# Kernel tuning notes

Measured on AMD Instinct MI355X. Metric: run time of the kernel, lower is better.

Reference implementation:

```python
import jax, jax.numpy as jnp
from jax import lax
import numpy as np

B, T, N, HORIZON = 64, 12, 512, 12
IN_DIM = 1; OUT_DIM = 1; YCOV = 1
RNN = 64; MEM_NUM = 20; MEM_DIM = 64; EMB = 10; CHEB_K = 3
DEC_DIM = RNN + MEM_DIM  # 128


def _xavier(key, shape):
    fan_in, fan_out = shape[0], shape[-1]
    std = float(np.sqrt(2.0 / (fan_in + fan_out)))
    return jax.random.normal(key, shape, dtype=jnp.float32) * std


def _cheb_feats(A, x, batched):
    mm = (lambda a, v: jnp.einsum('bnm,bmc->bnc', a, v)) if batched else (lambda a, v: jnp.einsum('nm,bmc->bnc', a, v))
    gs = [x, mm(A, x)]
    for _ in range(CHEB_K - 2):
        gs.append(2.0 * mm(A, gs[-1]) - gs[-2])
    return jnp.concatenate(gs, axis=-1)


def _agcn(x, A, W, b, batched):
    return _cheb_feats(A, x, batched) @ W + b


def _cell(x, state, A, Wg, bg, Wu, bu, batched):
    # AGCRN GRU cell
    hid = state.shape[-1]
    inp = jnp.concatenate([x, state], axis=-1)
    z_r = jax.nn.sigmoid(_agcn(inp, A, Wg, bg, batched))
    z, r = z_r[..., :hid], z_r[..., hid:]
    cand = jnp.concatenate([x, z * state], axis=-1)
    hc = jnp.tanh(_agcn(cand, A, Wu, bu, batched))
    return r * state + (1.0 - r) * hc


def _encode(x, A, Wg, bg, Wu, bu):
    # x: [B,T,N,C] -> last hidden state [B,N,RNN]
    xt = jnp.swapaxes(x, 0, 1)  # [T,B,N,C]
    init = jnp.zeros((x.shape[0], x.shape[2], RNN), x.dtype)
    def step(state, xt_):
        h = _cell(xt_, state, A, Wg, bg, Wu, bu, batched=False)
        return h, None
    h_t, _ = lax.scan(step, init, xt)
    return h_t


def _query_memory(h_t, Memory, Wq):
    q = h_t @ Wq                                   # [B,N,mem_dim]
    att = jax.nn.softmax(q @ Memory.T, axis=-1)    # [B,N,mem_num]
    value = att @ Memory                           # [B,N,mem_dim]
    _, ind = lax.top_k(att, 2)
    pos = Memory[ind[..., 0]]                      # [B,N,mem_dim]
    return value, pos


def setup_inputs() -> dict:
    key = jax.random.key(0)
    ks = jax.random.split(key, 20)
    x = jax.random.normal(ks[0], (B, T, N, IN_DIM), dtype=jnp.float32)
    x_cov = jax.random.normal(ks[1], (B, T, N, 1), dtype=jnp.float32)
    x_his = jax.random.normal(ks[2], (B, T, N, IN_DIM), dtype=jnp.float32)
    y_cov = jax.random.normal(ks[3], (B, HORIZON, N, YCOV), dtype=jnp.float32)
    a = jax.random.uniform(ks[4], (N, N), dtype=jnp.float32)
    adj = a / jnp.sum(a, axis=-1, keepdims=True)
    enc_in = IN_DIM + RNN
    dec_in = OUT_DIM + YCOV + DEC_DIM
    return {
        'x': x, 'x_cov': x_cov, 'x_his': x_his, 'y_cov': y_cov, 'adj': adj,
        'enc_gate_W': _xavier(ks[5], (CHEB_K * enc_in, 2 * RNN)),
        'enc_gate_b': jnp.zeros((2 * RNN,), jnp.float32),
        'enc_upd_W': _xavier(ks[6], (CHEB_K * enc_in, RNN)),
        'enc_upd_b': jnp.zeros((RNN,), jnp.float32),
        'dec_gate_W': _xavier(ks[7], (CHEB_K * dec_in, 2 * DEC_DIM)),
        'dec_gate_b': jnp.zeros((2 * DEC_DIM,), jnp.float32),
        'dec_upd_W': _xavier(ks[8], (CHEB_K * dec_in, DEC_DIM)),
        'dec_upd_b': jnp.zeros((DEC_DIM,), jnp.float32),
        'Memory': _xavier(ks[9], (MEM_NUM, MEM_DIM)),
        'Wq': _xavier(ks[10], (RNN, MEM_DIM)),
        'hyper_W': _xavier(ks[11], (DEC_DIM, EMB)),
        'hyper_b': jnp.zeros((EMB,), jnp.float32),
        'lat_W': _xavier(ks[12], (MEM_DIM, 1)),
        'lat_b': jnp.zeros((1,), jnp.float32),
        'proj_W': _xavier(ks[13], (DEC_DIM, OUT_DIM)),
        'proj_b': jnp.zeros((OUT_DIM,), jnp.float32),
    }


def reference(x, x_cov, x_his, y_cov, adj,
              enc_gate_W, enc_gate_b, enc_upd_W, enc_upd_b,
              dec_gate_W, dec_gate_b, dec_upd_W, dec_upd_b,
              Memory, Wq, hyper_W, hyper_b, lat_W, lat_b, proj_W, proj_b):
    # --- encoder on x and x_his (shared weights, single static support) ---
    h_t = _encode(x, adj, enc_gate_W, enc_gate_b, enc_upd_W, enc_upd_b)
    h_att, pos = _query_memory(h_t, Memory, Wq)
    h_his_t = _encode(x_his, adj, enc_gate_W, enc_gate_b, enc_upd_W, enc_upd_b)
    _, pos_his = _query_memory(h_his_t, Memory, Wq)
    # schema==1 latent distance head (sigmoid activation)
    latent_dis = jax.nn.sigmoid(((pos - pos_his) @ lat_W + lat_b)[..., 0])  # [B,N]
    # --- adaptive decoder support from hypernetwork ---
    h_aug = jnp.concatenate([h_t, h_att], axis=-1)          # [B,N,DEC_DIM]
    node_emb = h_aug @ hyper_W + hyper_b                    # [B,N,EMB]
    support = jax.nn.softmax(jax.nn.relu(jnp.einsum('bnc,bmc->bnm', node_emb, node_emb)), axis=-1)  # [B,N,N]
    # --- decoder rollout (inference path, no teacher forcing) ---
    go0 = jnp.zeros((x.shape[0], N, OUT_DIM), x.dtype)
    ycov_t = jnp.swapaxes(y_cov, 0, 1)  # [HORIZON,B,N,YCOV]
    def dec_step(carry, yc):
        go, h = carry
        xt = jnp.concatenate([go, yc], axis=-1)
        h = _cell(xt, h, support, dec_gate_W, dec_gate_b, dec_upd_W, dec_upd_b, batched=True)
        go = h @ proj_W + proj_b
        return (go, h), go
    _, outs = lax.scan(dec_step, (go0, h_aug), ycov_t)
    output = jnp.swapaxes(outs, 0, 1)  # [B,HORIZON,N,OUT_DIM]
    return output, latent_dis
```

## Files before the change

### kernel.cpp

```cpp
#include <hip/hip_runtime.h>
#include <hip/hip_bf16.h>


typedef __attribute__((ext_vector_type(8))) short s8v;
typedef __attribute__((ext_vector_type(4))) float f4v;
typedef __attribute__((ext_vector_type(4))) unsigned short u4v;

__device__ __forceinline__ float b2f(unsigned short u){
  union{unsigned int i; float f;} v; v.i = ((unsigned int)u)<<16; return v.f;
}
__device__ __forceinline__ unsigned short f2b(float f){
  union{float f; unsigned int i;} v; v.f = f;
  unsigned int r = v.i + 0x7fff + ((v.i >> 16) & 1);
  return (unsigned short)(r >> 16);
}

__global__ void k_zero16(uint4* p, int n){
  int i = blockIdx.x*256 + threadIdx.x;
  if (i < n) p[i] = make_uint4(0,0,0,0);
}


__global__ void k_reorderF(const float* __restrict__ W, float* __restrict__ Wr,
                           int HC, int NEX, int SEGW, int J){
  int idx = blockIdx.x*256 + threadIdx.x;
  int K = 3*SEGW;
  if (idx >= K*J) return;
  int k = idx / J, j = idx - k*J;
  int seg = k / SEGW, c = k - seg*SEGW;
  int CIN = HC + NEX;
  float v = 0.f;
  if (c < HC)       v = W[(size_t)(seg*CIN + NEX + c)*J + j];
  else if (c < CIN) v = W[(size_t)(seg*CIN + (c-HC))*J + j];
  Wr[(size_t)k*J + j] = v;
}

__global__ __launch_bounds__(256) void k_a2e(const float* __restrict__ A,
                                             float* __restrict__ A2e){
  __shared__ __align__(16) float As[32][132];
  __shared__ __align__(16) float Bs[32][132];
  int t = threadIdx.x;
  int r0 = (blockIdx.x & 3) * 128;
  int c0 = (blockIdx.x >> 2) * 128;
  int tr = t & 15, tc = t >> 4;
  float acc[8][8];
  #pragma unroll
  for (int i=0;i<8;i++)
    #pragma unroll
    for (int j=0;j<8;j++) acc[i][j]=0.f;
  for (int k0=0;k0<512;k0+=32){
    #pragma unroll
    for (int i=0;i<4;i++){
      int s = t + i*256;
      int k = s & 31, rq = s >> 5;
      const float* ap = A + (size_t)(r0 + rq*4)*512 + k0 + k;
      float4 v;
      v.x = ap[0]; v.y = ap[512]; v.z = ap[1024]; v.w = ap[1536];
      *(float4*)&As[k][rq*4] = v;
    }
    #pragma unroll
    for (int i=0;i<4;i++){
      int s = t + i*256;
      int k = s >> 5, cq = s & 31;
      float4 v = *(const float4*)(A + (size_t)(k0+k)*512 + c0 + cq*4);
      *(float4*)&Bs[k][cq*4] = v;
    }
    __syncthreads();
    #pragma unroll 8
    for (int k=0;k<32;k++){
      float a[8], b[8];
      *(float4*)&a[0] = *(const float4*)&As[k][tr*4];
      *(float4*)&a[4] = *(const float4*)&As[k][64+tr*4];
      *(float4*)&b[0] = *(const float4*)&Bs[k][tc*4];
      *(float4*)&b[4] = *(const float4*)&Bs[k][64+tc*4];
      #pragma unroll
      for (int i=0;i<8;i++)
        #pragma unroll
        for (int j=0;j<8;j++) acc[i][j] += a[i]*b[j];
    }
    __syncthreads();
  }
  #pragma unroll
  for (int i=0;i<8;i++){
    int r = r0 + (i<4 ? tr*4+i : 64+tr*4+i-4);
    #pragma unroll
    for (int j=0;j<8;j++){
      int c = c0 + (j<4 ? tc*4+j : 64+tc*4+j-4);
      A2e[(size_t)r*512 + c] = 2.f*acc[i][j] - (r==c ? 1.f : 0.f);
    }
  }
}

template<int MODE>
__global__ __launch_bounds__(256) void k_enc(
    const float* __restrict__ A, const float* __restrict__ A2e,
    const float* __restrict__ hsrc,
    const float* __restrict__ xa, const float* __restrict__ xb,
    int tstep, const float* __restrict__ Wr, const float* __restrict__ bias,
    float* __restrict__ zh, float* __restrict__ rbuf, float* __restrict__ henc)
{
  constexpr int J  = (MODE==0) ? 128 : 64;
  constexpr int TN = (MODE==0) ? 8 : 4;
  __shared__ __align__(16) float R1[4352];
  __shared__ __align__(16) float F0t[2][65][66];
  float (*sA)[68]   = (float(*)[68])(R1);
  float (*sA2)[68]  = (float(*)[68])(R1 + 1088);
  float (*sB0)[68]  = (float(*)[68])(R1 + 2176);
  float (*sB1)[68]  = (float(*)[68])(R1 + 3264);
  float (*G12h)[66] = (float(*)[66])(R1);
  const int t = threadIdx.x;
  const int z = blockIdx.x;
  const int rowblk = blockIdx.z;
  const int n0 = rowblk * 64;
  const int tr = t & 15, tc = t >> 4;
  const int xrow = t & 63, xmat = (t >> 6) & 1, xbb = t >> 7;
  const float* xp0 = xa + ((size_t)z*12 + tstep)*512;
  const float* xp1 = xb + ((size_t)z*12 + tstep)*512;

  float acc[2][2][4][4];
  #pragma unroll
  for (int m=0;m<2;m++)
    #pragma unroll
    for (int b=0;b<2;b++)
      #pragma unroll
      for (int i=0;i<4;i++)
        #pragma unroll
        for (int j=0;j<4;j++) acc[m][b][i][j]=0.f;
  float xacc = 0.f;

  for (int k0=0;k0<512;k0+=16){
    {
      int k = t & 15, rq = t >> 4;
      const float* ap  = A   + (size_t)(n0 + rq*4)*512 + k0 + k;
      const float* a2p = A2e + (size_t)(n0 + rq*4)*512 + k0 + k;
      float4 v, w;
      v.x = ap[0];  v.y = ap[512];  v.z = ap[1024];  v.w = ap[1536];
      w.x = a2p[0]; w.y = a2p[512]; w.z = a2p[1024]; w.w = a2p[1536];
      *(float4*)&sA[k][rq*4]  = v;
      *(float4*)&sA2[k][rq*4] = w;
    }
    {
      int k = t >> 4, cq = t & 15;
      *(float4*)&sB0[k][cq*4] = *(const float4*)(hsrc + (size_t)(z*512 + k0 + k)*64 + cq*4);
      *(float4*)&sB1[k][cq*4] = *(const float4*)(hsrc + (size_t)((z+64)*512 + k0 + k)*64 + cq*4);
    }
    if (t < 16)      sB0[t][64]    = xp0[k0 + t];
    else if (t < 32) sB1[t-16][64] = xp1[k0 + t - 16];
    __syncthreads();
    #pragma unroll 4
    for (int k=0;k<16;k++){
      float a1[4], a2[4], b0[4], b1[4];
      *(float4*)&a1[0] = *(const float4*)&sA[k][tr*4];
      *(float4*)&a2[0] = *(const float4*)&sA2[k][tr*4];
      *(float4*)&b0[0] = *(const float4*)&sB0[k][tc*4];
      *(float4*)&b1[0] = *(const float4*)&sB1[k][tc*4];
      #pragma unroll
      for (int i=0;i<4;i++)
        #pragma unroll
        for (int j=0;j<4;j++){
          acc[0][0][i][j] += a1[i]*b0[j];
          acc[0][1][i][j] += a1[i]*b1[j];
          acc[1][0][i][j] += a2[i]*b0[j];
          acc[1][1][i][j] += a2[i]*b1[j];
        }
      float am = xmat ? sA2[k][xrow] : sA[k][xrow];
      xacc += am * (xbb ? sB1[k][64] : sB0[k][64]);
    }
    if ((k0 >> 6) == rowblk){
      const int off = k0 & 63;
      for (int s=t; s<2080; s+=256){
        int sb = (s >= 1040) ? 1 : 0;
        int ss = s - sb*1040;
        int c = ss >> 4, kk = ss & 15;
        F0t[sb][c][off + kk] = sb ? sB1[kk][c] : sB0[kk][c];
      }
    }
    __syncthreads();
  }

  for (int bbi=0; bbi<2; bbi++){
    #pragma unroll
    for (int j=0;j<4;j++){
      float4 v;
      v.x = acc[0][bbi][0][j]; v.y = acc[0][bbi][1][j];
      v.z = acc[0][bbi][2][j]; v.w = acc[0][bbi][3][j];
      *(float4*)&G12h[tc*4 + j][tr*4] = v;
    }
    if (xbb == bbi && xmat == 0) G12h[64][xrow] = xacc;
    __syncthreads();

    float acc2[4][TN];
    #pragma unroll
    for (int i=0;i<4;i++)
      #pragma unroll
      for (int jj=0;jj<TN;jj++) acc2[i][jj]=0.f;
    const int j0 = tc*TN;

    #pragma unroll 4
    for (int c=0;c<65;c++){
      float a[4], w[TN];
      *(float4*)&a[0] = *(const float4*)&F0t[bbi][c][tr*4];
      #pragma unroll
      for (int q=0;q<TN;q+=4) *(float4*)&w[q] = *(const float4*)(Wr + (size_t)c*J + j0 + q);
      #pragma unroll
      for (int i=0;i<4;i++)
        #pragma unroll
        for (int jj=0;jj<TN;jj++) acc2[i][jj] += a[i]*w[jj];
    }
    #pragma unroll 4
    for (int c=0;c<65;c++){
      float a[4], w[TN];
      *(float4*)&a[0] = *(const float4*)&G12h[c][tr*4];
      #pragma unroll
      for (int q=0;q<TN;q+=4) *(float4*)&w[q] = *(const float4*)(Wr + (size_t)(68+c)*J + j0 + q);
      #pragma unroll
      for (int i=0;i<4;i++)
        #pragma unroll
        for (int jj=0;jj<TN;jj++) acc2[i][jj] += a[i]*w[jj];
    }
    __syncthreads();
    #pragma unroll
    for (int j=0;j<4;j++){
      float4 v;
      v.x = acc[1][bbi][0][j]; v.y = acc[1][bbi][1][j];
      v.z = acc[1][bbi][2][j]; v.w = acc[1][bbi][3][j];
      *(float4*)&G12h[tc*4 + j][tr*4] = v;
    }
    if (xbb == bbi && xmat == 1) G12h[64][xrow] = xacc;
    __syncthreads();
    #pragma unroll 4
    for (int c=0;c<65;c++){
      float a[4], w[TN];
      *(float4*)&a[0] = *(const float4*)&G12h[c][tr*4];
      #pragma unroll
      for (int q=0;q<TN;q+=4) *(float4*)&w[q] = *(const float4*)(Wr + (size_t)(136+c)*J + j0 + q);
      #pragma unroll
      for (int i=0;i<4;i++)
        #pragma unroll
        for (int jj=0;jj<TN;jj++) acc2[i][jj] += a[i]*w[jj];
    }

    float bj[TN];
    #pragma unroll
    for (int jj=0;jj<TN;jj++) bj[jj] = bias[j0+jj];
    const int gbase = (z + bbi*64)*512 + n0;
    #pragma unroll
    for (int i=0;i<4;i++){
      const int lr = tr*4 + i;
      const int row = gbase + lr;
      if (MODE == 0){
        float s[8];
        #pragma unroll
        for (int jj=0;jj<TN;jj++) s[jj] = 1.f/(1.f + __expf(-(acc2[i][jj] + bj[jj])));
        if (j0 < 64){
          float4 o0, o1;
          o0.x = s[0]*F0t[bbi][j0+0][lr]; o0.y = s[1]*F0t[bbi][j0+1][lr];
          o0.z = s[2]*F0t[bbi][j0+2][lr]; o0.w = s[3]*F0t[bbi][j0+3][lr];
          o1.x = s[4]*F0t[bbi][j0+4][lr]; o1.y = s[5]*F0t[bbi][j0+5][lr];
          o1.z = s[6]*F0t[bbi][j0+6][lr]; o1.w = s[7]*F0t[bbi][j0+7][lr];
          *(float4*)(zh + (size_t)row*64 + j0)     = o0;
          *(float4*)(zh + (size_t)row*64 + j0 + 4) = o1;
        } else {
          float4 o0, o1;
          o0.x=s[0]; o0.y=s[1]; o0.z=s[2]; o0.w=s[3];
          o1.x=s[4]; o1.y=s[5]; o1.z=s[6]; o1.w=s[7];
          *(float4*)(rbuf + (size_t)row*64 + j0 - 64) = o0;
          *(float4*)(rbuf + (size_t)row*64 + j0 - 60) = o1;
        }
      } else {
        float4 h4 = *(const float4*)(henc + (size_t)row*64 + j0);
        float4 r4 = *(const float4*)(rbuf + (size_t)row*64 + j0);
        float hv[4] = {h4.x,h4.y,h4.z,h4.w};
        float rv[4] = {r4.x,r4.y,r4.z,r4.w};
        float ov[4];
        #pragma unroll
        for (int jj=0;jj<4;jj++){
          float hc = 1.f - 2.f/(__expf(2.f*(acc2[i][jj] + bj[jj])) + 1.f);
          ov[jj] = rv[jj]*hv[jj] + (1.f - rv[jj])*hc;
        }
        float4 o; o.x=ov[0]; o.y=ov[1]; o.z=ov[2]; o.w=ov[3];
        *(float4*)(henc + (size_t)row*64 + j0) = o;
      }
    }
    __syncthreads();
  }
}


__global__ void k_reorderB(const float* __restrict__ W, unsigned short* __restrict__ Wr,
                           int HC, int NEX, int C, int KP, int J){
  int idx = blockIdx.x*256 + threadIdx.x;
  if (idx >= J*KP) return;
  int j = idx / KP, kp = idx - j*KP;
  float v = 0.f;
  if (kp < 3*C){
    int seg = kp / C, c = kp - seg*C;
    int CIN = HC + NEX;
    if (c < HC)       v = W[(size_t)(seg*CIN + NEX + c)*J + j];
    else if (c < CIN) v = W[(size_t)(seg*CIN + (c-HC))*J + j];
  }
  Wr[(size_t)j*KP + kp] = f2b(v);
}

__global__ __launch_bounds__(256) void k_sup2(const unsigned short* __restrict__ S,
                                              unsigned short* __restrict__ S2){
  __shared__ unsigned short Bs[128*40];
  const int t = threadIdx.x;
  const int w = t >> 6, L = t & 63, lm = L & 15, q = L >> 4;
  const int bb = blockIdx.z;
  const int n0 = blockIdx.x * 128;
  const int m0 = blockIdx.y * 128;
  const unsigned short* Sb = S + (size_t)bb * 262144;
  unsigned short* S2b = S2 + (size_t)bb * 262144;
  f4v acc[2][8];
  #pragma unroll
  for (int i=0;i<2;i++)
    #pragma unroll
    for (int j=0;j<8;j++)
      #pragma unroll
      for (int r=0;r<4;r++) acc[i][j][r] = 0.f;
  for (int k0=0;k0<512;k0+=32){
    #pragma unroll
    for (int i=0;i<2;i++){
      int s = t + i*256;
      int kk = s >> 4, mg = s & 15;
      s8v v = *(const s8v*)(Sb + (size_t)(k0+kk)*512 + m0 + mg*8);
      #pragma unroll
      for (int e=0;e<8;e++) Bs[(mg*8+e)*40 + kk] = ((unsigned short*)&v)[e];
    }
    __syncthreads();
    s8v a0 = *(const s8v*)(Sb + (size_t)(n0 + w*32 + lm)*512 + k0 + q*8);
    s8v a1 = *(const s8v*)(Sb + (size_t)(n0 + w*32 + 16 + lm)*512 + k0 + q*8);
    #pragma unroll
    for (int ct=0;ct<8;ct++){
      s8v b = *(const s8v*)&Bs[(ct*16+lm)*40 + q*8];
      acc[0][ct] = __builtin_amdgcn_mfma_f32_16x16x32_bf16(a0, b, acc[0][ct], 0,0,0);
      acc[1][ct] = __builtin_amdgcn_mfma_f32_16x16x32_bf16(a1, b, acc[1][ct], 0,0,0);
    }
    __syncthreads();
  }
  #pragma unroll
  for (int rt=0;rt<2;rt++){
    const int row = n0 + w*32 + rt*16 + q*4;
    #pragma unroll
    for (int ct=0;ct<8;ct++){
      const int col = m0 + ct*16 + lm;
      #pragma unroll
      for (int r=0;r<4;r++){
        float v = 2.f*acc[rt][ct][r] - ((row+r)==col ? 1.f : 0.f);
        S2b[(size_t)(row+r)*512 + col] = f2b(v);
      }
    }
  }
}

__global__ __launch_bounds__(256) void k_mmB2(
    const unsigned short* __restrict__ M1, const unsigned short* __restrict__ M2,
    unsigned short* fC, unsigned short* fR)
{
  constexpr int C = 144;
  __shared__ unsigned short Bs[C*40];
  const int t = threadIdx.x;
  const int w = t >> 6, L = t & 63, lm = L & 15, q = L >> 4;
  const int bb = blockIdx.z;
  const int n0 = blockIdx.x * 64;
  const unsigned short* M1b = M1 + (size_t)bb * 262144;
  const unsigned short* M2b = M2 + (size_t)bb * 262144;
  unsigned short* fCb = fC + (size_t)bb * 432 * 512;
  const unsigned short* Xb = fCb;
  unsigned short* O1 = fCb + (size_t)C * 512;
  unsigned short* O2 = fCb + (size_t)2 * C * 512;
  const int rw = n0 + w*16;

  f4v acc[2][9];
  #pragma unroll
  for (int i=0;i<2;i++)
    #pragma unroll
    for (int j=0;j<9;j++)
      #pragma unroll
      for (int r=0;r<4;r++) acc[i][j][r] = 0.f;

  s8v breg[3];
  const size_t ar = (size_t)(rw + lm)*512 + q*8;
  #pragma unroll
  for (int i=0;i<3;i++){
    int s = t + i*256;
    if (s < C*4) breg[i] = *(const s8v*)(Xb + (size_t)(s>>2)*512 + (s&3)*8);
  }
  s8v a1 = *(const s8v*)(M1b + ar);
  s8v a2 = *(const s8v*)(M2b + ar);

  for (int ks=0; ks<16; ks++){
    #pragma unroll
    for (int i=0;i<3;i++){
      int s = t + i*256;
      if (s < C*4) *(s8v*)&Bs[(s>>2)*40 + (s&3)*8] = breg[i];
    }
    __syncthreads();
    const int kn = (ks < 15) ? (ks+1)*32 : 0;
    #pragma unroll
    for (int i=0;i<3;i++){
      int s = t + i*256;
      if (s < C*4) breg[i] = *(const s8v*)(Xb + (size_t)(s>>2)*512 + kn + (s&3)*8);
    }
    s8v a1n = *(const s8v*)(M1b + ar + kn);
    s8v a2n = *(const s8v*)(M2b + ar + kn);
    #pragma unroll
    for (int ct=0; ct<9; ct++){
      s8v b = *(const s8v*)&Bs[(ct*16+lm)*40 + q*8];
      acc[0][ct] = __builtin_amdgcn_mfma_f32_16x16x32_bf16(a1, b, acc[0][ct], 0,0,0);
      acc[1][ct] = __builtin_amdgcn_mfma_f32_16x16x32_bf16(a2, b, acc[1][ct], 0,0,0);
    }
    __syncthreads();
    a1 = a1n; a2 = a2n;
  }
  const int m0 = rw + q*4;
  #pragma unroll
  for (int ct=0; ct<9; ct++){
    const int c = ct*16 + lm;
    u4v o1, o2;
    #pragma unroll
    for (int r=0;r<4;r++){ o1[r] = f2b(acc[0][ct][r]); o2[r] = f2b(acc[1][ct][r]); }
    *(u4v*)(O1 + (size_t)c*512 + m0) = o1;
    *(u4v*)(O2 + (size_t)c*512 + m0) = o2;
    const size_t rb = (size_t)(bb*512 + m0)*448;
    #pragma unroll
    for (int r=0;r<4;r++){
      fR[rb + (size_t)r*448 + 144 + c] = o1[r];
      fR[rb + (size_t)r*448 + 288 + c] = o2[r];
    }
  }
}

template<int KSTEPS, int JT16, int MODE, int HC>
__global__ __launch_bounds__(256) void k_gwB(
    unsigned short* fR, int KP,
    const unsigned short* __restrict__ Wr, const float* __restrict__ bias,
    unsigned short* fC, int C3,
    float* hC, float* rbuf)
{
  constexpr int JT = JT16*16;
  constexpr int BIT = JT*4/256;
  __shared__ unsigned short Bs[JT*40];
  const int t = threadIdx.x;
  const int w = t >> 6, L = t & 63, lm = L & 15, q = L >> 4;
  const int row0 = blockIdx.x * 128;
  const int j0 = blockIdx.y * JT;
  const int rw = row0 + w*32;

  f4v acc[2][JT16];
  #pragma unroll
  for (int i=0;i<2;i++)
    #pragma unroll
    for (int j=0;j<JT16;j++)
      #pragma unroll
      for (int r=0;r<4;r++) acc[i][j][r] = 0.f;

  s8v breg[BIT];
  const unsigned short* Wb = Wr + (size_t)j0*KP;
  const size_t ar0 = (size_t)(rw + lm)*KP + q*8;
  const size_t ar1 = (size_t)(rw + 16 + lm)*KP + q*8;

  #pragma unroll
  for (int i=0;i<BIT;i++){
    int s = t + i*256;
    breg[i] = *(const s8v*)(Wb + (size_t)(s>>2)*KP + (s&3)*8);
  }
  s8v a0 = *(const s8v*)(fR + ar0);
  s8v a1 = *(const s8v*)(fR + ar1);

  for (int ks=0; ks<KSTEPS; ks++){
    #pragma unroll
    for (int i=0;i<BIT;i++){
      int s = t + i*256;
      *(s8v*)&Bs[(s>>2)*40 + (s&3)*8] = breg[i];
    }
    __syncthreads();
    const int kn = (ks < KSTEPS-1) ? (ks+1)*32 : 0;
    #pragma unroll
    for (int i=0;i<BIT;i++){
      int s = t + i*256;
      breg[i] = *(const s8v*)(Wb + (size_t)(s>>2)*KP + kn + (s&3)*8);
    }
    s8v a0n = *(const s8v*)(fR + ar0 + kn);
    s8v a1n = *(const s8v*)(fR + ar1 + kn);
    #pragma unroll
    for (int ct=0; ct<JT16; ct++){
      s8v b = *(const s8v*)&Bs[(ct*16+lm)*40 + q*8];
      acc[0][ct] = __builtin_amdgcn_mfma_f32_16x16x32_bf16(a0, b, acc[0][ct], 0,0,0);
      acc[1][ct] = __builtin_amdgcn_mfma_f32_16x16x32_bf16(a1, b, acc[1][ct], 0,0,0);
    }
    __syncthreads();
    a0 = a0n; a1 = a1n;
  }
  #pragma unroll
  for (int rt=0; rt<2; rt++){
    const int m0 = rw + rt*16 + q*4;
    const int bb = m0 >> 9, n = m0 & 511;
    #pragma unroll
    for (int ct=0; ct<JT16; ct++){
      const int j = j0 + ct*16 + lm;
      const float bj = bias[j];
      if (MODE == 0){
        if (j < HC){
          f4v h4 = *(const f4v*)(hC + ((size_t)bb*HC + j)*512 + n);
          u4v o;
          #pragma unroll
          for (int r=0;r<4;r++){
            float s = 1.f/(1.f + __expf(-(acc[rt][ct][r] + bj)));
            float zh = s * h4[r];
            o[r] = f2b(zh);
            fR[(size_t)(m0+r)*KP + j] = o[r];
          }
          *(u4v*)(fC + ((size_t)bb*C3 + j)*512 + n) = o;
        } else {
          f4v rv;
          #pragma unroll
          for (int r=0;r<4;r++) rv[r] = 1.f/(1.f + __expf(-(acc[rt][ct][r] + bj)));
          *(f4v*)(rbuf + ((size_t)bb*HC + (j-HC))*512 + n) = rv;
        }
      } else {
        f4v h4 = *(const f4v*)(hC + ((size_t)bb*HC + j)*512 + n);
        f4v r4 = *(const f4v*)(rbuf + ((size_t)bb*HC + j)*512 + n);
        u4v o; f4v hn;
        #pragma unroll
        for (int r=0;r<4;r++){
          float e = __expf(2.f*(acc[rt][ct][r] + bj));
          float hc_ = 1.f - 2.f/(e + 1.f);
          hn[r] = r4[r]*h4[r] + (1.f - r4[r])*hc_;
          o[r] = f2b(hn[r]);
          fR[(size_t)(m0+r)*KP + j] = o[r];
        }
        *(f4v*)(hC + ((size_t)bb*HC + j)*512 + n) = hn;
        *(u4v*)(fC + ((size_t)bb*C3 + j)*512 + n) = o;
      }
    }
  }
}


__global__ void k_extras_dec(const float* __restrict__ yc,
    unsigned short* fR, unsigned short* fC, int tstep){
  int rr = blockIdx.x*256 + threadIdx.x;
  int bb = rr >> 9, n = rr & 511;
  unsigned short u = f2b(yc[((size_t)bb*12 + tstep)*512 + n]);
  fR[(size_t)rr*448 + 129] = u;
  fC[((size_t)bb*432 + 129)*512 + n] = u;
}
__global__ void k_fix_go(unsigned short* fR, unsigned short* fC){
  int rr = blockIdx.x*256 + threadIdx.x;
  int bb = rr >> 9, n = rr & 511;
  fR[(size_t)rr*448 + 128] = 0;
  fC[((size_t)bb*432 + 128)*512 + n] = 0;
}

__global__ __launch_bounds__(256) void k_query(const float* __restrict__ hR,
      const float* __restrict__ Wq, const float* __restrict__ Mem,
      float* __restrict__ hCd, unsigned short* fR, unsigned short* fC,
      int* __restrict__ it, int* __restrict__ ih){
  int sub = threadIdx.x >> 6, lane = threadIdx.x & 63;
  int row = blockIdx.x*4 + sub;
  __shared__ float sh[4][64], sq[4][64], ss[4][20];
  float hv = hR[(size_t)row*64 + lane];
  sh[sub][lane] = hv;
  __syncthreads();
  float qv = 0.f;
  for (int c=0;c<64;c++) qv += sh[sub][c]*Wq[c*64 + lane];
  sq[sub][lane] = qv;
  __syncthreads();
  if (lane < 20){
    float s = 0.f;
    for (int j=0;j<64;j++) s += sq[sub][j]*Mem[lane*64 + j];
    ss[sub][lane] = s;
  }
  __syncthreads();
  float mx = -1e30f; int am = 0;
  for (int m=0;m<20;m++){ float s = ss[sub][m]; if (s > mx){ mx = s; am = m; } }
  float sum = 0.f;
  for (int m=0;m<20;m++) sum += __expf(ss[sub][m]-mx);
  float inv = 1.f/sum;
  float v = 0.f;
  for (int m=0;m<20;m++) v += __expf(ss[sub][m]-mx)*inv*Mem[m*64 + lane];
  int bb = row >> 9, n = row & 511;
  if (bb < 64){
    hCd[((size_t)bb*128 + lane)*512 + n] = hv;
    hCd[((size_t)bb*128 + 64 + lane)*512 + n] = v;
    fR[(size_t)row*448 + lane] = f2b(hv);
    fR[(size_t)row*448 + 64 + lane] = f2b(v);
    fC[((size_t)bb*432 + lane)*512 + n] = f2b(hv);
    fC[((size_t)bb*432 + 64 + lane)*512 + n] = f2b(v);
    if (lane==0) it[row] = am;
  } else {
    if (lane==0) ih[row - 32768] = am;
  }
}

__global__ void k_latent(const int* __restrict__ it, const int* __restrict__ ih,
                         const float* __restrict__ Mem,
                         const float* __restrict__ lW, const float* __restrict__ lb,
                         float* __restrict__ outl){
  int row = blockIdx.x*256 + threadIdx.x;
  int i1 = it[row], i2 = ih[row];
  float a = lb[0];
  for (int c=0;c<64;c++) a += (Mem[i1*64+c]-Mem[i2*64+c])*lW[c];
  outl[row] = 1.f/(1.f + __expf(-a));
}

__global__ __launch_bounds__(256) void k_emb(const float* __restrict__ hCd,
    const float* __restrict__ hW, const float* __restrict__ hb, float* __restrict__ emb){
  __shared__ float sW[1280];
  int t = threadIdx.x;
  for (int s=t; s<1280; s+=256) sW[s] = hW[s];
  __syncthreads();
  int rr = blockIdx.x*256 + t;
  int bb = rr >> 9, n = rr & 511;
  float a[10];
  #pragma unroll
  for (int e=0;e<10;e++) a[e] = hb[e];
  for (int c=0;c<128;c++){
    float v = hCd[((size_t)bb*128 + c)*512 + n];
    #pragma unroll
    for (int e=0;e<10;e++) a[e] += v*sW[c*10+e];
  }
  #pragma unroll
  for (int e=0;e<10;e++) emb[(size_t)rr*10 + e] = a[e];
}

__global__ __launch_bounds__(256) void k_support(const float* __restrict__ emb,
                                                 unsigned short* __restrict__ sup){
  int b = blockIdx.x >> 9;
  int n = blockIdx.x & 511;
  int t = threadIdx.x;
  __shared__ float se[5120];
  __shared__ float red[8];
  for (int s = t; s < 5120; s += 256) se[s] = emb[(size_t)b*5120 + s];
  __syncthreads();
  float en[10];
  #pragma unroll
  for (int i=0;i<10;i++) en[i] = se[n*10+i];
  float s0=0.f, s1=0.f;
  #pragma unroll
  for (int i=0;i<10;i++){ s0 += en[i]*se[t*10+i]; s1 += en[i]*se[(t+256)*10+i]; }
  s0 = fmaxf(s0, 0.f); s1 = fmaxf(s1, 0.f);
  float mx = fmaxf(s0, s1);
  for (int o=32;o>0;o>>=1) mx = fmaxf(mx, __shfl_down(mx, o));
  if ((t&63)==0) red[t>>6] = mx;
  __syncthreads();
  mx = fmaxf(fmaxf(red[0],red[1]), fmaxf(red[2],red[3]));
  float e0 = __expf(s0-mx), e1 = __expf(s1-mx);
  float sm = e0 + e1;
  for (int o=32;o>0;o>>=1) sm += __shfl_down(sm, o);
  if ((t&63)==0) red[4+(t>>6)] = sm;
  __syncthreads();
  sm = red[4]+red[5]+red[6]+red[7];
  float inv = 1.f/sm;
  size_t base = ((size_t)b*512 + n)*512;
  sup[base + t]       = f2b(e0*inv);
  sup[base + t + 256] = f2b(e1*inv);
}

__global__ __launch_bounds__(256) void k_proj(const float* __restrict__ hCd,
    const float* __restrict__ pW, const float* __restrict__ pb,
    unsigned short* fR, unsigned short* fC, float* __restrict__ out, int tstep){
  __shared__ float sW[128];
  int t = threadIdx.x;
  if (t < 128) sW[t] = pW[t];
  __syncthreads();
  int rr = blockIdx.x*256 + t;
  int bb = rr >> 9, n = rr & 511;
  float a = pb[0];
  for (int c=0;c<128;c++) a += hCd[((size_t)bb*128 + c)*512 + n]*sW[c];
  out[((size_t)bb*12 + tstep)*512 + n] = a;
  unsigned short u = f2b(a);
  fR[(size_t)rr*448 + 128] = u;
  fC[((size_t)bb*432 + 128)*512 + n] = u;
}

extern "C" void kernel_launch(void* const* d_in, const int* in_sizes, int n_in,
                              void* d_out, int out_size, void* d_ws, size_t ws_size,
                              hipStream_t stream) {
  const float* x     = (const float*)d_in[0];
  const float* x_his = (const float*)d_in[2];
  const float* y_cov = (const float*)d_in[3];
  const float* adj   = (const float*)d_in[4];
  const float* egW   = (const float*)d_in[5];
  const float* egb   = (const float*)d_in[6];
  const float* euW   = (const float*)d_in[7];
  const float* eub   = (const float*)d_in[8];
  const float* dgW   = (const float*)d_in[9];
  const float* dgb   = (const float*)d_in[10];
  const float* duW   = (const float*)d_in[11];
  const float* dub   = (const float*)d_in[12];
  const float* Mem   = (const float*)d_in[13];
  const float* Wq    = (const float*)d_in[14];
  const float* hW    = (const float*)d_in[15];
  const float* hb    = (const float*)d_in[16];
  const float* lW    = (const float*)d_in[17];
  const float* lb    = (const float*)d_in[18];
  const float* pW    = (const float*)d_in[19];
  const float* pb    = (const float*)d_in[20];
  float* out  = (float*)d_out;
  float* outl = out + 393216;

  char* base = (char*)d_ws;
  size_t off = 0;
  auto alloc = [&](size_t bytes)->char*{
    char* p = base + off; off = (off + bytes + 255) & ~(size_t)255; return p;
  };
  unsigned short* sup  = (unsigned short*)alloc(33554432);
  unsigned short* sup2 = (unsigned short*)alloc(33554432);
  float* emb  = (float*)alloc(1310720);
  int*   it   = (int*)alloc(131072);
  int*   ih   = (int*)alloc(131072);
  float* henc = (float*)alloc(16777216);
  float* zhF  = (float*)alloc(16777216);
  float* hCd  = zhF;
  float* rbF  = (float*)alloc(16777216);
  unsigned short* fR = (unsigned short*)alloc(29360128);
  unsigned short* fC = (unsigned short*)alloc(28311552);
  float* a2e = (float*)alloc(1048576);
  float* wr_egF = (float*)alloc(104448);
  float* wr_euF = (float*)alloc(52224);
  unsigned short* wr_dg = (unsigned short*)alloc(229376);
  unsigned short* wr_du = (unsigned short*)alloc(114688);
  if (ws_size < off) return;

  k_zero16<<<4096,256,0,stream>>>((uint4*)henc, 1048576);
  k_zero16<<<7168,256,0,stream>>>((uint4*)fR, 1835008);
  k_zero16<<<6912,256,0,stream>>>((uint4*)fC, 1769472);
  k_a2e<<<16,256,0,stream>>>(adj, a2e);
  k_reorderF<<<102,256,0,stream>>>(egW, wr_egF, 64,1,68,128);
  k_reorderF<<< 51,256,0,stream>>>(euW, wr_euF, 64,1,68,64);
  k_reorderB<<<448,256,0,stream>>>(dgW, wr_dg, 128,2,144,448,256);
  k_reorderB<<<224,256,0,stream>>>(duW, wr_du, 128,2,144,448,128);

  for (int t = 0; t < 12; t++){
    k_enc<0><<<dim3(64,1,8),256,0,stream>>>(adj, a2e, henc, x, x_his, t,
                                            wr_egF, egb, zhF, rbF, nullptr);
    k_enc<1><<<dim3(64,1,8),256,0,stream>>>(adj, a2e, zhF, x, x_his, t,
                                            wr_euF, eub, nullptr, rbF, henc);
  }

  k_query<<<16384,256,0,stream>>>(henc, Wq, Mem, hCd, fR, fC, it, ih);
  k_latent<<<128,256,0,stream>>>(it, ih, Mem, lW, lb, outl);
  k_emb<<<128,256,0,stream>>>(hCd, hW, hb, emb);
  k_support<<<32768,256,0,stream>>>(emb, sup);
  k_sup2<<<dim3(4,4,64),256,0,stream>>>(sup, sup2);
  k_fix_go<<<128,256,0,stream>>>(fR, fC);

  for (int t = 0; t < 12; t++){
    k_extras_dec<<<128,256,0,stream>>>(y_cov, fR, fC, t);
    k_mmB2<<<dim3(8,1,64),256,0,stream>>>(sup, sup2, fC, fR);
    k_gwB<14,16,0,128><<<dim3(256,1),256,0,stream>>>(fR, 448, wr_dg, dgb, fC, 432, hCd, rbF);
    k_mmB2<<<dim3(8,1,64),256,0,stream>>>(sup, sup2, fC, fR);
    k_gwB<14,8,1,128><<<dim3(256,1),256,0,stream>>>(fR, 448, wr_du, dub, fC, 432, hCd, rbF);
    k_proj<<<128,256,0,stream>>>(hCd, pW, pb, fR, fC, out, t);
  }
}
```

Measured before the change: 6.101 ms.

## Split encoder kernel to one batch per block, doubling grid size

The encoder kernel previously processed two batch slices (x and x_his) per block, sharing the adjacency tiles between them. Now each block handles a single batch slice, and the grid doubles from 64x8 to 128x8 blocks. This lowers per-thread accumulator registers and shared memory, which should raise occupancy and spread the work over more CUs. The cost is that the A and A2e tiles are loaded from global memory twice as often.

```diff
diff --git a/kernel.cpp b/kernel.cpp
--- a/kernel.cpp
+++ b/kernel.cpp
@@ -102,30 +102,27 @@
   constexpr int J  = (MODE==0) ? 128 : 64;
   constexpr int TN = (MODE==0) ? 8 : 4;
   __shared__ __align__(16) float R1[4352];
-  __shared__ __align__(16) float F0t[2][65][66];
+  __shared__ __align__(16) float F0t[65][66];
   float (*sA)[68]   = (float(*)[68])(R1);
   float (*sA2)[68]  = (float(*)[68])(R1 + 1088);
-  float (*sB0)[68]  = (float(*)[68])(R1 + 2176);
-  float (*sB1)[68]  = (float(*)[68])(R1 + 3264);
+  float (*sB)[68]   = (float(*)[68])(R1 + 2176);
   float (*G12h)[66] = (float(*)[66])(R1);
   const int t = threadIdx.x;
-  const int z = blockIdx.x;
+  const int bb = blockIdx.x;
   const int rowblk = blockIdx.z;
   const int n0 = rowblk * 64;
   const int tr = t & 15, tc = t >> 4;
-  const int xrow = t & 63, xmat = (t >> 6) & 1, xbb = t >> 7;
-  const float* xp0 = xa + ((size_t)z*12 + tstep)*512;
-  const float* xp1 = xb + ((size_t)z*12 + tstep)*512;
-
-  float acc[2][2][4][4];
+  const int xrow = t & 63, xmat = (t >> 6) & 1;
+  const float* xp = (bb < 64) ? (xa + ((size_t)bb*12 + tstep)*512)
+                              : (xb + ((size_t)(bb-64)*12 + tstep)*512);
+
+  float acc[2][4][4];
   #pragma unroll
   for (int m=0;m<2;m++)
     #pragma unroll
-    for (int b=0;b<2;b++)
-      #pragma unroll
-      for (int i=0;i<4;i++)
-        #pragma unroll
-        for (int j=0;j<4;j++) acc[m][b][i][j]=0.f;
+    for (int i=0;i<4;i++)
+      #pragma unroll
+      for (int j=0;j<4;j++) acc[m][i][j]=0.f;
   float xacc = 0.f;
 
   for (int k0=0;k0<512;k0+=16){
@@ -141,148 +138,138 @@
     }
     {
       int k = t >> 4, cq = t & 15;
-      *(float4*)&sB0[k][cq*4] = *(const float4*)(hsrc + (size_t)(z*512 + k0 + k)*64 + cq*4);
-      *(float4*)&sB1[k][cq*4] = *(const float4*)(hsrc + (size_t)((z+64)*512 + k0 + k)*64 + cq*4);
-    }
-    if (t < 16)      sB0[t][64]    = xp0[k0 + t];
-    else if (t < 32) sB1[t-16][64] = xp1[k0 + t - 16];
+      *(float4*)&sB[k][cq*4] = *(const float4*)(hsrc + (size_t)(bb*512 + k0 + k)*64 + cq*4);
+    }
+    if (t < 16) sB[t][64] = xp[k0 + t];
     __syncthreads();
     #pragma unroll 4
     for (int k=0;k<16;k++){
-      float a1[4], a2[4], b0[4], b1[4];
+      float a1[4], a2[4], b[4];
       *(float4*)&a1[0] = *(const float4*)&sA[k][tr*4];
       *(float4*)&a2[0] = *(const float4*)&sA2[k][tr*4];
-      *(float4*)&b0[0] = *(const float4*)&sB0[k][tc*4];
-      *(float4*)&b1[0] = *(const float4*)&sB1[k][tc*4];
+      *(float4*)&b[0]  = *(const float4*)&sB[k][tc*4];
       #pragma unroll
       for (int i=0;i<4;i++)
         #pragma unroll
         for (int j=0;j<4;j++){
-          acc[0][0][i][j] += a1[i]*b0[j];
-          acc[0][1][i][j] += a1[i]*b1[j];
-          acc[1][0][i][j] += a2[i]*b0[j];
-          acc[1][1][i][j] += a2[i]*b1[j];
+          acc[0][i][j] += a1[i]*b[j];
+          acc[1][i][j] += a2[i]*b[j];
         }
       float am = xmat ? sA2[k][xrow] : sA[k][xrow];
-      xacc += am * (xbb ? sB1[k][64] : sB0[k][64]);
+      xacc += am * sB[k][64];
     }
     if ((k0 >> 6) == rowblk){
       const int off = k0 & 63;
-      for (int s=t; s<2080; s+=256){
-        int sb = (s >= 1040) ? 1 : 0;
-        int ss = s - sb*1040;
-        int c = ss >> 4, kk = ss & 15;
-        F0t[sb][c][off + kk] = sb ? sB1[kk][c] : sB0[kk][c];
+      for (int s=t; s<1040; s+=256){
+        int c = s >> 4, kk = s & 15;
+        F0t[c][off + kk] = sB[kk][c];
       }
     }
     __syncthreads();
   }
 
-  for (int bbi=0; bbi<2; bbi++){
-    #pragma unroll
-    for (int j=0;j<4;j++){
-      float4 v;
-      v.x = acc[0][bbi][0][j]; v.y = acc[0][bbi][1][j];
-      v.z = acc[0][bbi][2][j]; v.w = acc[0][bbi][3][j];
-      *(float4*)&G12h[tc*4 + j][tr*4] = v;
-    }
-    if (xbb == bbi && xmat == 0) G12h[64][xrow] = xacc;
-    __syncthreads();
-
-    float acc2[4][TN];
+  #pragma unroll
+  for (int j=0;j<4;j++){
+    float4 v;
+    v.x = acc[0][0][j]; v.y = acc[0][1][j];
+    v.z = acc[0][2][j]; v.w = acc[0][3][j];
+    *(float4*)&G12h[tc*4 + j][tr*4] = v;
+  }
+  if (t < 64) G12h[64][xrow] = xacc;
+  __syncthreads();
+
+  float acc2[4][TN];
+  #pragma unroll
+  for (int i=0;i<4;i++)
+    #pragma unroll
+    for (int jj=0;jj<TN;jj++) acc2[i][jj]=0.f;
+  const int j0 = tc*TN;
+
+  #pragma unroll 4
+  for (int c=0;c<65;c++){
+    float a[4], w[TN];
+    *(float4*)&a[0] = *(const float4*)&F0t[c][tr*4];
+    #pragma unroll
+    for (int q=0;q<TN;q+=4) *(float4*)&w[q] = *(const float4*)(Wr + (size_t)c*J + j0 + q);
     #pragma unroll
     for (int i=0;i<4;i++)
       #pragma unroll
-      for (int jj=0;jj<TN;jj++) acc2[i][jj]=0.f;
-    const int j0 = tc*TN;
-
-    #pragma unroll 4
-    for (int c=0;c<65;c++){
-      float a[4], w[TN];
-      *(float4*)&a[0] = *(const float4*)&F0t[bbi][c][tr*4];
-      #pragma unroll
-      for (int q=0;q<TN;q+=4) *(float4*)&w[q] = *(const float4*)(Wr + (size_t)c*J + j0 + q);
-      #pragma unroll
-      for (int i=0;i<4;i++)
-        #pragma unroll
-        for (int jj=0;jj<TN;jj++) acc2[i][jj] += a[i]*w[jj];
-    }
-    #pragma unroll 4
-    for (int c=0;c<65;c++){
-      float a[4], w[TN];
-      *(float4*)&a[0] = *(const float4*)&G12h[c][tr*4];
-      #pragma unroll
-      for (int q=0;q<TN;q+=4) *(float4*)&w[q] = *(const float4*)(Wr + (size_t)(68+c)*J + j0 + q);
-      #pragma unroll
-      for (int i=0;i<4;i++)
-        #pragma unroll
-        for (int jj=0;jj<TN;jj++) acc2[i][jj] += a[i]*w[jj];
-    }
-    __syncthreads();
-    #pragma unroll
-    for (int j=0;j<4;j++){
-      float4 v;
-      v.x = acc[1][bbi][0][j]; v.y = acc[1][bbi][1][j];
-      v.z = acc[1][bbi][2][j]; v.w = acc[1][bbi][3][j];
-      *(float4*)&G12h[tc*4 + j][tr*4] = v;
-    }
-    if (xbb == bbi && xmat == 1) G12h[64][xrow] = xacc;
-    __syncthreads();
-    #pragma unroll 4
-    for (int c=0;c<65;c++){
-      float a[4], w[TN];
-      *(float4*)&a[0] = *(const float4*)&G12h[c][tr*4];
-      #pragma unroll
-      for (int q=0;q<TN;q+=4) *(float4*)&w[q] = *(const float4*)(Wr + (size_t)(136+c)*J + j0 + q);
-      #pragma unroll
-      for (int i=0;i<4;i++)
-        #pragma unroll
-        for (int jj=0;jj<TN;jj++) acc2[i][jj] += a[i]*w[jj];
-    }
-
-    float bj[TN];
-    #pragma unroll
-    for (int jj=0;jj<TN;jj++) bj[jj] = bias[j0+jj];
-    const int gbase = (z + bbi*64)*512 + n0;
-    #pragma unroll
-    for (int i=0;i<4;i++){
-      const int lr = tr*4 + i;
-      const int row = gbase + lr;
-      if (MODE == 0){
-        float s[8];
-        #pragma unroll
-        for (int jj=0;jj<TN;jj++) s[jj] = 1.f/(1.f + __expf(-(acc2[i][jj] + bj[jj])));
-        if (j0 < 64){
-          float4 o0, o1;
-          o0.x = s[0]*F0t[bbi][j0+0][lr]; o0.y = s[1]*F0t[bbi][j0+1][lr];
-          o0.z = s[2]*F0t[bbi][j0+2][lr]; o0.w = s[3]*F0t[bbi][j0+3][lr];
-          o1.x = s[4]*F0t[bbi][j0+4][lr]; o1.y = s[5]*F0t[bbi][j0+5][lr];
-          o1.z = s[6]*F0t[bbi][j0+6][lr]; o1.w = s[7]*F0t[bbi][j0+7][lr];
-          *(float4*)(zh + (size_t)row*64 + j0)     = o0;
-          *(float4*)(zh + (size_t)row*64 + j0 + 4) = o1;
-        } else {
-          float4 o0, o1;
-          o0.x=s[0]; o0.y=s[1]; o0.z=s[2]; o0.w=s[3];
-          o1.x=s[4]; o1.y=s[5]; o1.z=s[6]; o1.w=s[7];
-          *(float4*)(rbuf + (size_t)row*64 + j0 - 64) = o0;
-          *(float4*)(rbuf + (size_t)row*64 + j0 - 60) = o1;
-        }
+      for (int jj=0;jj<TN;jj++) acc2[i][jj] += a[i]*w[jj];
+  }
+  #pragma unroll 4
+  for (int c=0;c<65;c++){
+    float a[4], w[TN];
+    *(float4*)&a[0] = *(const float4*)&G12h[c][tr*4];
+    #pragma unroll
+    for (int q=0;q<TN;q+=4) *(float4*)&w[q] = *(const float4*)(Wr + (size_t)(68+c)*J + j0 + q);
+    #pragma unroll
+    for (int i=0;i<4;i++)
+      #pragma unroll
+      for (int jj=0;jj<TN;jj++) acc2[i][jj] += a[i]*w[jj];
+  }
+  __syncthreads();
+  #pragma unroll
+  for (int j=0;j<4;j++){
+    float4 v;
+    v.x = acc[1][0][j]; v.y = acc[1][1][j];
+    v.z = acc[1][2][j]; v.w = acc[1][3][j];
+    *(float4*)&G12h[tc*4 + j][tr*4] = v;
+  }
+  if (t >= 64 && t < 128) G12h[64][xrow] = xacc;
+  __syncthreads();
+  #pragma unroll 4
+  for (int c=0;c<65;c++){
+    float a[4], w[TN];
+    *(float4*)&a[0] = *(const float4*)&G12h[c][tr*4];
+    #pragma unroll
+    for (int q=0;q<TN;q+=4) *(float4*)&w[q] = *(const float4*)(Wr + (size_t)(136+c)*J + j0 + q);
+    #pragma unroll
+    for (int i=0;i<4;i++)
+      #pragma unroll
+      for (int jj=0;jj<TN;jj++) acc2[i][jj] += a[i]*w[jj];
+  }
+
+  float bj[TN];
+  #pragma unroll
+  for (int jj=0;jj<TN;jj++) bj[jj] = bias[j0+jj];
+  const int gbase = bb*512 + n0;
+  #pragma unroll
+  for (int i=0;i<4;i++){
+    const int lr = tr*4 + i;
+    const int row = gbase + lr;
+    if (MODE == 0){
+      float s[8];
+      #pragma unroll
+      for (int jj=0;jj<TN;jj++) s[jj] = 1.f/(1.f + __expf(-(acc2[i][jj] + bj[jj])));
+      if (j0 < 64){
+        float4 o0, o1;
+        o0.x = s[0]*F0t[j0+0][lr]; o0.y = s[1]*F0t[j0+1][lr];
+        o0.z = s[2]*F0t[j0+2][lr]; o0.w = s[3]*F0t[j0+3][lr];
+        o1.x = s[4]*F0t[j0+4][lr]; o1.y = s[5]*F0t[j0+5][lr];
+        o1.z = s[6]*F0t[j0+6][lr]; o1.w = s[7]*F0t[j0+7][lr];
+        *(float4*)(zh + (size_t)row*64 + j0)     = o0;
+        *(float4*)(zh + (size_t)row*64 + j0 + 4) = o1;
       } else {
-        float4 h4 = *(const float4*)(henc + (size_t)row*64 + j0);
-        float4 r4 = *(const float4*)(rbuf + (size_t)row*64 + j0);
-        float hv[4] = {h4.x,h4.y,h4.z,h4.w};
-        float rv[4] = {r4.x,r4.y,r4.z,r4.w};
-        float ov[4];
-        #pragma unroll
-        for (int jj=0;jj<4;jj++){
-          float hc = 1.f - 2.f/(__expf(2.f*(acc2[i][jj] + bj[jj])) + 1.f);
-          ov[jj] = rv[jj]*hv[jj] + (1.f - rv[jj])*hc;
-        }
-        float4 o; o.x=ov[0]; o.y=ov[1]; o.z=ov[2]; o.w=ov[3];
-        *(float4*)(henc + (size_t)row*64 + j0) = o;
+        float4 o0, o1;
+        o0.x=s[0]; o0.y=s[1]; o0.z=s[2]; o0.w=s[3];
+        o1.x=s[4]; o1.y=s[5]; o1.z=s[6]; o1.w=s[7];
+        *(float4*)(rbuf + (size_t)row*64 + j0 - 64) = o0;
+        *(float4*)(rbuf + (size_t)row*64 + j0 - 60) = o1;
       }
-    }
-    __syncthreads();
+    } else {
+      float4 h4 = *(const float4*)(henc + (size_t)row*64 + j0);
+      float4 r4 = *(const float4*)(rbuf + (size_t)row*64 + j0);
+      float hv[4] = {h4.x,h4.y,h4.z,h4.w};
+      float rv[4] = {r4.x,r4.y,r4.z,r4.w};
+      float ov[4];
+      #pragma unroll
+      for (int jj=0;jj<4;jj++){
+        float hc = 1.f - 2.f/(__expf(2.f*(acc2[i][jj] + bj[jj])) + 1.f);
+        ov[jj] = rv[jj]*hv[jj] + (1.f - rv[jj])*hc;
+      }
+      float4 o; o.x=ov[0]; o.y=ov[1]; o.z=ov[2]; o.w=ov[3];
+      *(float4*)(henc + (size_t)row*64 + j0) = o;
+    }
   }
 }
 
@@ -735,10 +722,10 @@
   k_reorderB<<<224,256,0,stream>>>(duW, wr_du, 128,2,144,448,128);
 
   for (int t = 0; t < 12; t++){
-    k_enc<0><<<dim3(64,1,8),256,0,stream>>>(adj, a2e, henc, x, x_his, t,
-                                            wr_egF, egb, zhF, rbF, nullptr);
-    k_enc<1><<<dim3(64,1,8),256,0,stream>>>(adj, a2e, zhF, x, x_his, t,
-                                            wr_euF, eub, nullptr, rbF, henc);
+    k_enc<0><<<dim3(128,1,8),256,0,stream>>>(adj, a2e, henc, x, x_his, t,
+                                             wr_egF, egb, zhF, rbF, nullptr);
+    k_enc<1><<<dim3(128,1,8),256,0,stream>>>(adj, a2e, zhF, x, x_his, t,
+                                             wr_euF, eub, nullptr, rbF, henc);
   }
 
   k_query<<<16384,256,0,stream>>>(henc, Wq, Mem, hCd, fR, fC, it, ih);
```

Result: no change. 6.169 ms (+1.1%).
